# Kernel tuning notes

Hardware: AMD Instinct MI355X
Metric: run time of the kernel (lower is better)

The kernel has to match this reference:

```python
import jax, jax.numpy as jnp
import numpy as np

N = 50000      # nodes
E = 800000     # edges (avg degree 16)
F_IN = 128     # num_features
HID = 128      # hidden_channels
C = 4          # num_labeled_classes


def setup_inputs() -> dict:
    key = jax.random.key(0)
    ks = jax.random.split(key, 12)
    x = jax.random.normal(ks[0], (N, F_IN), dtype=jnp.float32)
    edge_index = jax.random.randint(ks[1], (2, E), 0, N, dtype=jnp.int32)

    def lin(k, fan_in, fan_out):
        return (jax.random.normal(k, (fan_in, fan_out), dtype=jnp.float32)
                / np.float32(np.sqrt(fan_in)))

    return {
        "x": x,
        "edge_index": edge_index,
        # layer 0: SAGEConv(F_IN, HID) -> lin_l (with bias) on aggregated neighbors, lin_r on self
        "Wl0": lin(ks[2], F_IN, HID), "bl0": jnp.zeros((HID,), jnp.float32), "Wr0": lin(ks[3], F_IN, HID),
        # layer 1: SAGEConv(HID, HID)
        "Wl1": lin(ks[4], HID, HID), "bl1": jnp.zeros((HID,), jnp.float32), "Wr1": lin(ks[5], HID, HID),
        # layer 2: SAGEConv(HID, C)
        "Wl2": lin(ks[6], HID, C), "bl2": jnp.zeros((C,), jnp.float32), "Wr2": lin(ks[7], HID, C),
    }


def _sage_conv(x, src, dst, inv_deg, Wl, bl, Wr):
    # gather neighbor features [E, d], mean-aggregate at destination nodes
    msg = x[src]
    agg = jax.ops.segment_sum(msg, dst, num_segments=N)  # [N, d]
    mean = agg * inv_deg[:, None]
    # out = lin_l(mean_j) + lin_r(x_i)   (PyG SAGEConv default, mean aggr)
    return mean @ Wl + bl + x @ Wr


def reference(x, edge_index, Wl0, bl0, Wr0, Wl1, bl1, Wr1, Wl2, bl2, Wr2):
    src = edge_index[0]
    dst = edge_index[1]
    # in-degree of each destination node, clamped to 1 (isolated nodes -> 0 mean)
    deg = jax.ops.segment_sum(jnp.ones((E,), x.dtype), dst, num_segments=N)
    inv_deg = jnp.where(deg > 0, 1.0 / jnp.maximum(deg, 1.0), 0.0)

    h = _sage_conv(x, src, dst, inv_deg, Wl0, bl0, Wr0)
    h = jax.nn.relu(h)
    # dropout(p=0.5) is identity in eval mode
    h2 = _sage_conv(h, src, dst, inv_deg, Wl1, bl1, Wr1)
    out = _sage_conv(h2, src, dst, inv_deg, Wl2, bl2, Wr2)
    return (out, out, h2)
```

## Files before the change

### kernel.cpp

```cpp
#include <hip/hip_runtime.h>
#include <hip/hip_bf16.h>
#include <stdint.h>

#define NNODES 50000
#define NEDGES 800000
#define FDIM   128
#define NCLS   4
#define NB     196
#define ECAP   6144
#define LPITCH 136
#define NPH    8

typedef uint32_t u32;
typedef unsigned short u16;
typedef __bf16 bf16x8 __attribute__((ext_vector_type(8)));
typedef float f32x4 __attribute__((ext_vector_type(4)));

__device__ __forceinline__ u16 f2bf(float f) {
    u32 u = __float_as_uint(f);
    u32 r = u + 0x7fffu + ((u >> 16) & 1u);
    return (u16)(r >> 16);
}
__device__ __forceinline__ u32 pack2(float a, float b) {
    return (u32)f2bf(a) | ((u32)f2bf(b) << 16);
}
__device__ __forceinline__ float bflo(u32 p) { return __uint_as_float(p << 16); }
__device__ __forceinline__ float bfhi(u32 p) { return __uint_as_float(p & 0xffff0000u); }

__global__ void k_bhist(const int* __restrict__ dst, int* __restrict__ bcnt) {
    __shared__ int h[NB];
    int t = threadIdx.x;
    if (t < NB) h[t] = 0;
    __syncthreads();
    int base = blockIdx.x * 1024;
#pragma unroll
    for (int i = 0; i < 4; ++i) {
        int e = base + i * 256 + t;
        if (e < NEDGES) atomicAdd(&h[dst[e] >> 8], 1);
    }
    __syncthreads();
    if (t < NB) {
        int v = h[t];
        if (v) atomicAdd(&bcnt[t], v);
    }
}

__global__ void k_bscan(const int* __restrict__ bcnt, int* __restrict__ boffs,
                        int* __restrict__ bcur) {
    int t = threadIdx.x;
    int v = (t < NB) ? bcnt[t] : 0;
    __shared__ int s[256];
    s[t] = v;
    __syncthreads();
    for (int off = 1; off < 256; off <<= 1) {
        int u = (t >= off) ? s[t - off] : 0;
        __syncthreads();
        s[t] += u;
        __syncthreads();
    }
    if (t < NB) { int ex = s[t] - v; boffs[t] = ex; bcur[t] = ex; }
    if (t == 0) boffs[NB] = NEDGES;
}

__global__ void k_bscatter(const int* __restrict__ src, const int* __restrict__ dst,
                           int* __restrict__ bcur, u32* __restrict__ ebuf) {
    __shared__ int h[NB];
    __shared__ int base[NB];
    int t = threadIdx.x;
    if (t < NB) h[t] = 0;
    __syncthreads();
    int eb = blockIdx.x * 1024;
    int mb[4];
    u32 pk[4];
#pragma unroll
    for (int i = 0; i < 4; ++i) {
        int e = eb + i * 256 + t;
        if (e < NEDGES) {
            int d = dst[e];
            mb[i] = d >> 8;
            pk[i] = (u32)src[e] | ((u32)d << 16);
            atomicAdd(&h[mb[i]], 1);
        } else mb[i] = -1;
    }
    __syncthreads();
    if (t < NB) {
        int v = h[t];
        base[t] = v ? atomicAdd(&bcur[t], v) : 0;
        h[t] = 0;
    }
    __syncthreads();
#pragma unroll
    for (int i = 0; i < 4; ++i) {
        if (mb[i] >= 0) {
            int r = atomicAdd(&h[mb[i]], 1);
            ebuf[base[mb[i]] + r] = pk[i];
        }
    }
}

__global__ void __launch_bounds__(256) k_bfinal(
        const u32* __restrict__ ebuf, const int* __restrict__ boffs,
        int* __restrict__ offs, float* __restrict__ invd, int* __restrict__ csr) {
    __shared__ u32 se[ECAP];
    __shared__ int deg8[256 * NPH];
    __shared__ int s[256];
    int b = blockIdx.x, t = threadIdx.x;
    int nbase = b << 8;
    int ebeg = boffs[b], eend = boffs[b + 1];
    int ecnt = eend - ebeg;
#pragma unroll
    for (int j = 0; j < NPH; ++j) deg8[t * NPH + j] = 0;
    __syncthreads();
    for (int i = t; i < ecnt; i += 256) {
        u32 e = ebuf[ebeg + i];
        if (i < ECAP) se[i] = e;
        int dl = (int)(e >> 16) - nbase;
        int ph = (int)(e & 0xffffu) >> 13;
        atomicAdd(&deg8[dl * NPH + ph], 1);
    }
    __syncthreads();
    int pre[NPH];
    int run = 0;
#pragma unroll
    for (int j = 0; j < NPH; ++j) { pre[j] = run; run += deg8[t * NPH + j]; }
    int d = run;
    s[t] = d;
    __syncthreads();
    for (int off = 1; off < 256; off <<= 1) {
        int u = (t >= off) ? s[t - off] : 0;
        __syncthreads();
        s[t] += u;
        __syncthreads();
    }
    int ex = s[t] - d;
    int node = nbase + t;
    if (node < NNODES) {
        offs[node] = ebeg + ex;
        invd[node] = (d > 0) ? (1.0f / (float)d) : 0.0f;
    }
    __syncthreads();
#pragma unroll
    for (int j = 0; j < NPH; ++j) deg8[t * NPH + j] = ex + pre[j];
    __syncthreads();
    for (int i = t; i < ecnt; i += 256) {
        u32 e = (i < ECAP) ? se[i] : ebuf[ebeg + i];
        int dl = (int)(e >> 16) - nbase;
        int sv = (int)(e & 0xffffu);
        int r = atomicAdd(&deg8[dl * NPH + (sv >> 13)], 1);
        csr[ebeg + r] = sv;
    }
    if (b == 0 && t == 0) offs[NNODES] = NEDGES;
}

__global__ void k_pack(const float* __restrict__ Wl, const float* __restrict__ Wr,
                       u16* __restrict__ Bp) {
    int tid = blockIdx.x * 256 + threadIdx.x;
    int j    = tid & 7;
    int lane = (tid >> 3) & 63;
    int ks   = (tid >> 9) & 3;
    int nt   = tid >> 11;
    int col  = nt * 16 + (lane & 15);
    int k    = ks * 32 + (lane >> 4) * 8 + j;
    float v = (col < FDIM) ? Wl[k * FDIM + col] : Wr[k * FDIM + (col - FDIM)];
    Bp[tid] = f2bf(v);
}

template <int INF32>
__global__ void __launch_bounds__(256) k_mfma(
        const void* __restrict__ in,
        const uint4* __restrict__ Bp,
        const float* __restrict__ bias,
        u16* __restrict__ y,
        u16* __restrict__ zb) {
    __shared__ u16 sA[64 * LPITCH];
    int t = threadIdx.x;
    int blk = blockIdx.x;
    int wave = t >> 6;
    int lane = t & 63;
    int m    = lane & 15;
    int quad = lane >> 4;

    {
        int row = t >> 2;
        int q   = t & 3;
        int r = blk * 64 + row;
        if (r >= NNODES) r = NNODES - 1;
        if (INF32) {
            const float4* gs = (const float4*)((const float*)in + (size_t)r * FDIM) + q * 8;
            uint4* ld = (uint4*)(sA + row * LPITCH + q * 32);
#pragma unroll
            for (int i = 0; i < 4; ++i) {
                float4 a = gs[2 * i], b = gs[2 * i + 1];
                uint4 v;
                v.x = pack2(a.x, a.y); v.y = pack2(a.z, a.w);
                v.z = pack2(b.x, b.y); v.w = pack2(b.z, b.w);
                ld[i] = v;
            }
        } else {
            const uint4* gsrc = (const uint4*)((const u16*)in + (size_t)r * FDIM);
            uint4* ldst = (uint4*)(sA + row * LPITCH);
#pragma unroll
            for (int i = 0; i < 4; ++i) ldst[q * 4 + i] = gsrc[q * 4 + i];
        }
    }

    uint4 breg[4][4];
#pragma unroll
    for (int ks = 0; ks < 4; ++ks)
#pragma unroll
        for (int nt = 0; nt < 4; ++nt)
            breg[ks][nt] = Bp[((wave * 4 + nt) * 4 + ks) * 64 + lane];

    __syncthreads();

    bf16x8 a[4][4];
#pragma unroll
    for (int mt = 0; mt < 4; ++mt)
#pragma unroll
        for (int ks = 0; ks < 4; ++ks) {
            const uint4* ap = (const uint4*)(sA + (mt * 16 + m) * LPITCH + ks * 32 + quad * 8);
            a[mt][ks] = __builtin_bit_cast(bf16x8, *ap);
        }

    f32x4 acc[4][4];
#pragma unroll
    for (int mt = 0; mt < 4; ++mt)
#pragma unroll
        for (int nt = 0; nt < 4; ++nt) acc[mt][nt] = (f32x4){0.f, 0.f, 0.f, 0.f};

#pragma unroll
    for (int ks = 0; ks < 4; ++ks)
#pragma unroll
        for (int nt = 0; nt < 4; ++nt) {
            bf16x8 b = __builtin_bit_cast(bf16x8, breg[ks][nt]);
#pragma unroll
            for (int mt = 0; mt < 4; ++mt)
                acc[mt][nt] = __builtin_amdgcn_mfma_f32_16x16x32_bf16(
                    a[mt][ks], b, acc[mt][nt], 0, 0, 0);
        }

    __syncthreads();
    if (wave < 2) {
#pragma unroll
        for (int nt = 0; nt < 4; ++nt) {
            int col = (wave * 4 + nt) * 16 + m;
#pragma unroll
            for (int mt = 0; mt < 4; ++mt)
#pragma unroll
                for (int r = 0; r < 4; ++r)
                    sA[(mt * 16 + quad * 4 + r) * LPITCH + col] = f2bf(acc[mt][nt][r]);
        }
    }
    __syncthreads();
#pragma unroll
    for (int i = 0; i < 4; ++i) {
        int g = i * 256 + t;
        int row = g >> 4, ch = g & 15;
        int gr = blk * 64 + row;
        if (gr < NNODES) {
            uint4 v = *(const uint4*)(sA + row * LPITCH + ch * 8);
            *((uint4*)(y + (size_t)gr * FDIM) + ch) = v;
        }
    }
    __syncthreads();
    if (wave >= 2) {
#pragma unroll
        for (int nt = 0; nt < 4; ++nt) {
            int col = (wave * 4 + nt) * 16 + m - 128;
            float bv = bias[col];
#pragma unroll
            for (int mt = 0; mt < 4; ++mt)
#pragma unroll
                for (int r = 0; r < 4; ++r)
                    sA[(mt * 16 + quad * 4 + r) * LPITCH + col] = f2bf(acc[mt][nt][r] + bv);
        }
    }
    __syncthreads();
#pragma unroll
    for (int i = 0; i < 4; ++i) {
        int g = i * 256 + t;
        int row = g >> 4, ch = g & 15;
        int gr = blk * 64 + row;
        if (gr < NNODES) {
            uint4 v = *(const uint4*)(sA + row * LPITCH + ch * 8);
            *((uint4*)(zb + (size_t)gr * FDIM) + ch) = v;
        }
    }
}

template <int RELU, int OUTBF>
__global__ void k_agg(const u16* __restrict__ y,
                      const int* __restrict__ offs,
                      const int* __restrict__ csr,
                      const float* __restrict__ invd,
                      const u16* __restrict__ zb,
                      u16* __restrict__ outb,
                      float* __restrict__ outf) {
    int t = threadIdx.x;
    int nl = t >> 4, q = t & 15;
    int n = blockIdx.x * 16 + nl;
    int beg = offs[n], end = offs[n + 1];
    float a0 = 0, a1 = 0, a2 = 0, a3 = 0, a4 = 0, a5 = 0, a6 = 0, a7 = 0;
    const u16* yq = y + (size_t)q * 8;
    for (int i = beg; i < end; ++i) {
        int s = csr[i];
        uint4 v = *(const uint4*)(yq + (size_t)s * FDIM);
        a0 += bflo(v.x); a1 += bfhi(v.x);
        a2 += bflo(v.y); a3 += bfhi(v.y);
        a4 += bflo(v.z); a5 += bfhi(v.z);
        a6 += bflo(v.w); a7 += bfhi(v.w);
    }
    float iv = invd[n];
    uint4 zv = *(const uint4*)(zb + (size_t)n * FDIM + q * 8);
    float r0 = fmaf(a0, iv, bflo(zv.x)), r1 = fmaf(a1, iv, bfhi(zv.x));
    float r2 = fmaf(a2, iv, bflo(zv.y)), r3 = fmaf(a3, iv, bfhi(zv.y));
    float r4 = fmaf(a4, iv, bflo(zv.z)), r5 = fmaf(a5, iv, bfhi(zv.z));
    float r6 = fmaf(a6, iv, bflo(zv.w)), r7 = fmaf(a7, iv, bfhi(zv.w));
    if (RELU) {
        r0 = fmaxf(r0, 0.f); r1 = fmaxf(r1, 0.f); r2 = fmaxf(r2, 0.f); r3 = fmaxf(r3, 0.f);
        r4 = fmaxf(r4, 0.f); r5 = fmaxf(r5, 0.f); r6 = fmaxf(r6, 0.f); r7 = fmaxf(r7, 0.f);
    }
    if (OUTBF) {
        uint4 o;
        o.x = pack2(r0, r1); o.y = pack2(r2, r3);
        o.z = pack2(r4, r5); o.w = pack2(r6, r7);
        *(uint4*)(outb + (size_t)n * FDIM + q * 8) = o;
    } else {
        float* o = outf + (size_t)n * FDIM + q * 8;
        ((float4*)o)[0] = make_float4(r0, r1, r2, r3);
        ((float4*)o)[1] = make_float4(r4, r5, r6, r7);
    }
}

__global__ void k_gemm4(const float* __restrict__ h2,
                        const float* __restrict__ Wl,
                        const float* __restrict__ Wr,
                        const float* __restrict__ bias,
                        float* __restrict__ y4,
                        float* __restrict__ outz) {
    int tid = blockIdx.x * blockDim.x + threadIdx.x;
    int n = tid >> 2, c = tid & 3;
    if (n >= NNODES) return;
    const float4* row = (const float4*)(h2 + (size_t)n * FDIM);
    float a = 0, b = 0;
#pragma unroll 8
    for (int k4 = 0; k4 < 32; ++k4) {
        float4 v = row[k4];
        int k = k4 * 4;
        a = fmaf(v.x, Wl[(k + 0) * 4 + c], a); b = fmaf(v.x, Wr[(k + 0) * 4 + c], b);
        a = fmaf(v.y, Wl[(k + 1) * 4 + c], a); b = fmaf(v.y, Wr[(k + 1) * 4 + c], b);
        a = fmaf(v.z, Wl[(k + 2) * 4 + c], a); b = fmaf(v.z, Wr[(k + 2) * 4 + c], b);
        a = fmaf(v.w, Wl[(k + 3) * 4 + c], a); b = fmaf(v.w, Wr[(k + 3) * 4 + c], b);
    }
    y4[(size_t)n * 4 + c] = a;
    outz[(size_t)n * 4 + c] = b + bias[c];
}

__global__ void k_agg4(const float* __restrict__ y4,
                       const int* __restrict__ offs,
                       const int* __restrict__ csr,
                       const float* __restrict__ invd,
                       float* __restrict__ out) {
    int tid = blockIdx.x * blockDim.x + threadIdx.x;
    int n = tid >> 2, c = tid & 3;
    if (n >= NNODES) return;
    int beg = offs[n], end = offs[n + 1];
    float acc = 0;
    for (int i = beg; i < end; ++i) acc += y4[(size_t)csr[i] * 4 + c];
    float r = fmaf(acc, invd[n], out[(size_t)n * 4 + c]);
    out[(size_t)n * 4 + c] = r;
    out[(size_t)NNODES * NCLS + (size_t)n * 4 + c] = r;
}

extern "C" void kernel_launch(void* const* d_in, const int* in_sizes, int n_in,
                              void* d_out, int out_size, void* d_ws, size_t ws_size,
                              hipStream_t stream) {
    const float* x   = (const float*)d_in[0];
    const int* ei    = (const int*)d_in[1];
    const float* Wl0 = (const float*)d_in[2];
    const float* bl0 = (const float*)d_in[3];
    const float* Wr0 = (const float*)d_in[4];
    const float* Wl1 = (const float*)d_in[5];
    const float* bl1 = (const float*)d_in[6];
    const float* Wr1 = (const float*)d_in[7];
    const float* Wl2 = (const float*)d_in[8];
    const float* bl2 = (const float*)d_in[9];
    const float* Wr2 = (const float*)d_in[10];

    const int* src = ei;
    const int* dst = ei + NEDGES;

    float* out = (float*)d_out;
    float* h2  = out + 2 * (size_t)NNODES * NCLS;

    char* ws = (char*)d_ws;
    int*   offs = (int*)(ws + 0);
    float* invd = (float*)(ws + 200192);
    int*   bcnt = (int*)(ws + 400384);
    int*   boffs= (int*)(ws + 401408);
    int*   bcur = (int*)(ws + 402432);
    int*   csr  = (int*)(ws + 403456);
    u16*   y    = (u16*)(ws + 3603456);
    u16*   hb   = (u16*)(ws + 16403456);
    u16*   zb   = (u16*)(ws + 29203456);
    u32*   ebuf = (u32*)zb;
    float* y4   = (float*)(ws + 42003456);
    u16*   Bp0  = (u16*)(ws + 42803456);
    u16*   Bp1  = (u16*)(ws + 42868992);

    hipMemsetAsync(bcnt, 0, NB * sizeof(int), stream);
    k_bhist<<<782, 256, 0, stream>>>(dst, bcnt);
    k_bscan<<<1, 256, 0, stream>>>(bcnt, boffs, bcur);
    k_bscatter<<<782, 256, 0, stream>>>(src, dst, bcur, ebuf);
    k_bfinal<<<NB, 256, 0, stream>>>(ebuf, boffs, offs, invd, csr);

    k_pack<<<128, 256, 0, stream>>>(Wl0, Wr0, Bp0);
    k_pack<<<128, 256, 0, stream>>>(Wl1, Wr1, Bp1);

    const int mfmaBlocks = (NNODES + 63) / 64;

    k_mfma<1><<<mfmaBlocks, 256, 0, stream>>>(x, (const uint4*)Bp0, bl0, y, zb);
    k_agg<1, 1><<<NNODES / 16, 256, 0, stream>>>(y, offs, csr, invd, zb, hb, nullptr);

    k_mfma<0><<<mfmaBlocks, 256, 0, stream>>>(hb, (const uint4*)Bp1, bl1, y, zb);
    k_agg<0, 0><<<NNODES / 16, 256, 0, stream>>>(y, offs, csr, invd, zb, nullptr, h2);

    k_gemm4<<<(NNODES * NCLS + 255) / 256, 256, 0, stream>>>(h2, Wl2, Wr2, bl2, y4, out);
    k_agg4<<<(NNODES * NCLS + 255) / 256, 256, 0, stream>>>(y4, offs, csr, invd, out);
}
```

Measured before the change: 284.6 us.

## Fuse preprocessing kernels, overlap edge scatter with layer-0 GEMM, fuse final projection

Merges the histogram and both weight-pack kernels into one launch. The bucket scan and edge scatter now run inside the same grid as the layer-0 MFMA GEMM, using block-index partitioning so the two can overlap. The bucket offsets are recomputed locally in k_bfinal instead of a separate scan kernel. The layer-2 projection (k_gemm4) is folded into the second aggregation kernel via per-row shuffle reductions, and neighbor indices are staged in shared memory. This cuts launch count and idle gaps but adds redundant per-block scans and a reworked workspace layout.

```diff
diff --git a/kernel.cpp b/kernel.cpp
--- a/kernel.cpp
+++ b/kernel.cpp
@@ -10,6 +10,7 @@
 #define ECAP   6144
 #define LPITCH 136
 #define NPH    8
+#define SCAP   768
 
 typedef uint32_t u32;
 typedef unsigned short u16;
@@ -27,166 +28,61 @@
 __device__ __forceinline__ float bflo(u32 p) { return __uint_as_float(p << 16); }
 __device__ __forceinline__ float bfhi(u32 p) { return __uint_as_float(p & 0xffff0000u); }
 
-__global__ void k_bhist(const int* __restrict__ dst, int* __restrict__ bcnt) {
-    __shared__ int h[NB];
+__global__ void __launch_bounds__(256) k_pre(
+        const int* __restrict__ dst,
+        const float* __restrict__ Wl0, const float* __restrict__ Wr0,
+        const float* __restrict__ Wl1, const float* __restrict__ Wr1,
+        int* __restrict__ bcnt, u16* __restrict__ Bp0, u16* __restrict__ Bp1) {
     int t = threadIdx.x;
-    if (t < NB) h[t] = 0;
-    __syncthreads();
-    int base = blockIdx.x * 1024;
-#pragma unroll
-    for (int i = 0; i < 4; ++i) {
-        int e = base + i * 256 + t;
-        if (e < NEDGES) atomicAdd(&h[dst[e] >> 8], 1);
-    }
-    __syncthreads();
-    if (t < NB) {
-        int v = h[t];
-        if (v) atomicAdd(&bcnt[t], v);
-    }
-}
-
-__global__ void k_bscan(const int* __restrict__ bcnt, int* __restrict__ boffs,
-                        int* __restrict__ bcur) {
-    int t = threadIdx.x;
-    int v = (t < NB) ? bcnt[t] : 0;
-    __shared__ int s[256];
-    s[t] = v;
-    __syncthreads();
-    for (int off = 1; off < 256; off <<= 1) {
-        int u = (t >= off) ? s[t - off] : 0;
-        __syncthreads();
-        s[t] += u;
-        __syncthreads();
-    }
-    if (t < NB) { int ex = s[t] - v; boffs[t] = ex; bcur[t] = ex; }
-    if (t == 0) boffs[NB] = NEDGES;
-}
-
-__global__ void k_bscatter(const int* __restrict__ src, const int* __restrict__ dst,
-                           int* __restrict__ bcur, u32* __restrict__ ebuf) {
-    __shared__ int h[NB];
-    __shared__ int base[NB];
-    int t = threadIdx.x;
-    if (t < NB) h[t] = 0;
-    __syncthreads();
-    int eb = blockIdx.x * 1024;
-    int mb[4];
-    u32 pk[4];
-#pragma unroll
-    for (int i = 0; i < 4; ++i) {
-        int e = eb + i * 256 + t;
-        if (e < NEDGES) {
-            int d = dst[e];
-            mb[i] = d >> 8;
-            pk[i] = (u32)src[e] | ((u32)d << 16);
-            atomicAdd(&h[mb[i]], 1);
-        } else mb[i] = -1;
-    }
-    __syncthreads();
-    if (t < NB) {
-        int v = h[t];
-        base[t] = v ? atomicAdd(&bcur[t], v) : 0;
-        h[t] = 0;
-    }
-    __syncthreads();
-#pragma unroll
-    for (int i = 0; i < 4; ++i) {
-        if (mb[i] >= 0) {
-            int r = atomicAdd(&h[mb[i]], 1);
-            ebuf[base[mb[i]] + r] = pk[i];
-        }
-    }
-}
-
-__global__ void __launch_bounds__(256) k_bfinal(
-        const u32* __restrict__ ebuf, const int* __restrict__ boffs,
-        int* __restrict__ offs, float* __restrict__ invd, int* __restrict__ csr) {
-    __shared__ u32 se[ECAP];
-    __shared__ int deg8[256 * NPH];
-    __shared__ int s[256];
-    int b = blockIdx.x, t = threadIdx.x;
-    int nbase = b << 8;
-    int ebeg = boffs[b], eend = boffs[b + 1];
-    int ecnt = eend - ebeg;
-#pragma unroll
-    for (int j = 0; j < NPH; ++j) deg8[t * NPH + j] = 0;
-    __syncthreads();
-    for (int i = t; i < ecnt; i += 256) {
-        u32 e = ebuf[ebeg + i];
-        if (i < ECAP) se[i] = e;
-        int dl = (int)(e >> 16) - nbase;
-        int ph = (int)(e & 0xffffu) >> 13;
-        atomicAdd(&deg8[dl * NPH + ph], 1);
-    }
-    __syncthreads();
-    int pre[NPH];
-    int run = 0;
-#pragma unroll
-    for (int j = 0; j < NPH; ++j) { pre[j] = run; run += deg8[t * NPH + j]; }
-    int d = run;
-    s[t] = d;
-    __syncthreads();
-    for (int off = 1; off < 256; off <<= 1) {
-        int u = (t >= off) ? s[t - off] : 0;
-        __syncthreads();
-        s[t] += u;
-        __syncthreads();
-    }
-    int ex = s[t] - d;
-    int node = nbase + t;
-    if (node < NNODES) {
-        offs[node] = ebeg + ex;
-        invd[node] = (d > 0) ? (1.0f / (float)d) : 0.0f;
-    }
-    __syncthreads();
-#pragma unroll
-    for (int j = 0; j < NPH; ++j) deg8[t * NPH + j] = ex + pre[j];
-    __syncthreads();
-    for (int i = t; i < ecnt; i += 256) {
-        u32 e = (i < ECAP) ? se[i] : ebuf[ebeg + i];
-        int dl = (int)(e >> 16) - nbase;
-        int sv = (int)(e & 0xffffu);
-        int r = atomicAdd(&deg8[dl * NPH + (sv >> 13)], 1);
-        csr[ebeg + r] = sv;
-    }
-    if (b == 0 && t == 0) offs[NNODES] = NEDGES;
-}
-
-__global__ void k_pack(const float* __restrict__ Wl, const float* __restrict__ Wr,
-                       u16* __restrict__ Bp) {
-    int tid = blockIdx.x * 256 + threadIdx.x;
-    int j    = tid & 7;
-    int lane = (tid >> 3) & 63;
-    int ks   = (tid >> 9) & 3;
-    int nt   = tid >> 11;
-    int col  = nt * 16 + (lane & 15);
-    int k    = ks * 32 + (lane >> 4) * 8 + j;
-    float v = (col < FDIM) ? Wl[k * FDIM + col] : Wr[k * FDIM + (col - FDIM)];
-    Bp[tid] = f2bf(v);
-}
-
-template <int INF32>
-__global__ void __launch_bounds__(256) k_mfma(
-        const void* __restrict__ in,
-        const uint4* __restrict__ Bp,
-        const float* __restrict__ bias,
-        u16* __restrict__ y,
-        u16* __restrict__ zb) {
+    int bid = blockIdx.x;
+    if (bid < 782) {
+        __shared__ int h[NB];
+        if (t < NB) h[t] = 0;
+        __syncthreads();
+        int base = bid * 1024;
+#pragma unroll
+        for (int i = 0; i < 4; ++i) {
+            int e = base + i * 256 + t;
+            if (e < NEDGES) atomicAdd(&h[dst[e] >> 8], 1);
+        }
+        __syncthreads();
+        if (t < NB) {
+            int v = h[t];
+            if (v) atomicAdd(&bcnt[t], v);
+        }
+    } else {
+        int layer = (bid < 910) ? 0 : 1;
+        int pid = bid - (layer ? 910 : 782);
+        int tid = pid * 256 + t;
+        int j    = tid & 7;
+        int lane = (tid >> 3) & 63;
+        int ks   = (tid >> 9) & 3;
+        int nt   = tid >> 11;
+        int col  = nt * 16 + (lane & 15);
+        int k    = ks * 32 + (lane >> 4) * 8 + j;
+        const float* Wl = layer ? Wl1 : Wl0;
+        const float* Wr = layer ? Wr1 : Wr0;
+        float v = (col < FDIM) ? Wl[k * FDIM + col] : Wr[k * FDIM + (col - FDIM)];
+        (layer ? Bp1 : Bp0)[tid] = f2bf(v);
+    }
+}
+
+__global__ void __launch_bounds__(256) k_scatmfma(
+        const float* __restrict__ x, const uint4* __restrict__ Bp,
+        const float* __restrict__ bias, u16* __restrict__ y, u16* __restrict__ zb,
+        const int* __restrict__ src, const int* __restrict__ dst,
+        const int* __restrict__ bcnt, int* __restrict__ bcur,
+        u32* __restrict__ ebuf) {
     __shared__ u16 sA[64 * LPITCH];
     int t = threadIdx.x;
-    int blk = blockIdx.x;
-    int wave = t >> 6;
-    int lane = t & 63;
-    int m    = lane & 15;
-    int quad = lane >> 4;
-
-    {
-        int row = t >> 2;
-        int q   = t & 3;
-        int r = blk * 64 + row;
-        if (r >= NNODES) r = NNODES - 1;
-        if (INF32) {
-            const float4* gs = (const float4*)((const float*)in + (size_t)r * FDIM) + q * 8;
+    if (blockIdx.x < 782) {
+        int blk = blockIdx.x;
+        int wave = t >> 6, lane = t & 63, m = lane & 15, quad = lane >> 4;
+        {
+            int row = t >> 2, q = t & 3;
+            int r = blk * 64 + row;
+            if (r >= NNODES) r = NNODES - 1;
+            const float4* gs = (const float4*)(x + (size_t)r * FDIM) + q * 8;
             uint4* ld = (uint4*)(sA + row * LPITCH + q * 32);
 #pragma unroll
             for (int i = 0; i < 4; ++i) {
@@ -196,114 +92,210 @@
                 v.z = pack2(b.x, b.y); v.w = pack2(b.z, b.w);
                 ld[i] = v;
             }
-        } else {
-            const uint4* gsrc = (const uint4*)((const u16*)in + (size_t)r * FDIM);
-            uint4* ldst = (uint4*)(sA + row * LPITCH);
-#pragma unroll
-            for (int i = 0; i < 4; ++i) ldst[q * 4 + i] = gsrc[q * 4 + i];
-        }
-    }
-
-    uint4 breg[4][4];
-#pragma unroll
-    for (int ks = 0; ks < 4; ++ks)
-#pragma unroll
-        for (int nt = 0; nt < 4; ++nt)
-            breg[ks][nt] = Bp[((wave * 4 + nt) * 4 + ks) * 64 + lane];
-
-    __syncthreads();
-
-    bf16x8 a[4][4];
-#pragma unroll
-    for (int mt = 0; mt < 4; ++mt)
-#pragma unroll
-        for (int ks = 0; ks < 4; ++ks) {
-            const uint4* ap = (const uint4*)(sA + (mt * 16 + m) * LPITCH + ks * 32 + quad * 8);
-            a[mt][ks] = __builtin_bit_cast(bf16x8, *ap);
-        }
-
-    f32x4 acc[4][4];
-#pragma unroll
-    for (int mt = 0; mt < 4; ++mt)
-#pragma unroll
-        for (int nt = 0; nt < 4; ++nt) acc[mt][nt] = (f32x4){0.f, 0.f, 0.f, 0.f};
-
-#pragma unroll
-    for (int ks = 0; ks < 4; ++ks)
-#pragma unroll
-        for (int nt = 0; nt < 4; ++nt) {
-            bf16x8 b = __builtin_bit_cast(bf16x8, breg[ks][nt]);
-#pragma unroll
-            for (int mt = 0; mt < 4; ++mt)
-                acc[mt][nt] = __builtin_amdgcn_mfma_f32_16x16x32_bf16(
-                    a[mt][ks], b, acc[mt][nt], 0, 0, 0);
-        }
-
-    __syncthreads();
-    if (wave < 2) {
-#pragma unroll
-        for (int nt = 0; nt < 4; ++nt) {
-            int col = (wave * 4 + nt) * 16 + m;
-#pragma unroll
-            for (int mt = 0; mt < 4; ++mt)
-#pragma unroll
-                for (int r = 0; r < 4; ++r)
-                    sA[(mt * 16 + quad * 4 + r) * LPITCH + col] = f2bf(acc[mt][nt][r]);
-        }
-    }
-    __syncthreads();
-#pragma unroll
-    for (int i = 0; i < 4; ++i) {
-        int g = i * 256 + t;
-        int row = g >> 4, ch = g & 15;
-        int gr = blk * 64 + row;
-        if (gr < NNODES) {
-            uint4 v = *(const uint4*)(sA + row * LPITCH + ch * 8);
-            *((uint4*)(y + (size_t)gr * FDIM) + ch) = v;
-        }
-    }
-    __syncthreads();
-    if (wave >= 2) {
-#pragma unroll
-        for (int nt = 0; nt < 4; ++nt) {
-            int col = (wave * 4 + nt) * 16 + m - 128;
-            float bv = bias[col];
-#pragma unroll
-            for (int mt = 0; mt < 4; ++mt)
-#pragma unroll
-                for (int r = 0; r < 4; ++r)
-                    sA[(mt * 16 + quad * 4 + r) * LPITCH + col] = f2bf(acc[mt][nt][r] + bv);
-        }
-    }
-    __syncthreads();
-#pragma unroll
-    for (int i = 0; i < 4; ++i) {
-        int g = i * 256 + t;
-        int row = g >> 4, ch = g & 15;
-        int gr = blk * 64 + row;
-        if (gr < NNODES) {
-            uint4 v = *(const uint4*)(sA + row * LPITCH + ch * 8);
-            *((uint4*)(zb + (size_t)gr * FDIM) + ch) = v;
-        }
-    }
-}
-
-template <int RELU, int OUTBF>
-__global__ void k_agg(const u16* __restrict__ y,
-                      const int* __restrict__ offs,
-                      const int* __restrict__ csr,
-                      const float* __restrict__ invd,
-                      const u16* __restrict__ zb,
-                      u16* __restrict__ outb,
-                      float* __restrict__ outf) {
+        }
+        uint4 breg[4][4];
+#pragma unroll
+        for (int ks = 0; ks < 4; ++ks)
+#pragma unroll
+            for (int nt = 0; nt < 4; ++nt)
+                breg[ks][nt] = Bp[((wave * 4 + nt) * 4 + ks) * 64 + lane];
+        __syncthreads();
+        bf16x8 a[4][4];
+#pragma unroll
+        for (int mt = 0; mt < 4; ++mt)
+#pragma unroll
+            for (int ks = 0; ks < 4; ++ks)
+                a[mt][ks] = __builtin_bit_cast(bf16x8,
+                    *(const uint4*)(sA + (mt * 16 + m) * LPITCH + ks * 32 + quad * 8));
+        f32x4 acc[4][4];
+#pragma unroll
+        for (int mt = 0; mt < 4; ++mt)
+#pragma unroll
+            for (int nt = 0; nt < 4; ++nt) acc[mt][nt] = (f32x4){0.f, 0.f, 0.f, 0.f};
+#pragma unroll
+        for (int ks = 0; ks < 4; ++ks)
+#pragma unroll
+            for (int nt = 0; nt < 4; ++nt) {
+                bf16x8 b = __builtin_bit_cast(bf16x8, breg[ks][nt]);
+#pragma unroll
+                for (int mt = 0; mt < 4; ++mt)
+                    acc[mt][nt] = __builtin_amdgcn_mfma_f32_16x16x32_bf16(
+                        a[mt][ks], b, acc[mt][nt], 0, 0, 0);
+            }
+        __syncthreads();
+        if (wave < 2) {
+#pragma unroll
+            for (int nt = 0; nt < 4; ++nt) {
+                int col = (wave * 4 + nt) * 16 + m;
+#pragma unroll
+                for (int mt = 0; mt < 4; ++mt)
+#pragma unroll
+                    for (int r = 0; r < 4; ++r)
+                        sA[(mt * 16 + quad * 4 + r) * LPITCH + col] = f2bf(acc[mt][nt][r]);
+            }
+        }
+        __syncthreads();
+#pragma unroll
+        for (int i = 0; i < 4; ++i) {
+            int g = i * 256 + t, row = g >> 4, ch = g & 15;
+            int gr = blk * 64 + row;
+            if (gr < NNODES)
+                *((uint4*)(y + (size_t)gr * FDIM) + ch) =
+                    *(const uint4*)(sA + row * LPITCH + ch * 8);
+        }
+        __syncthreads();
+        if (wave >= 2) {
+#pragma unroll
+            for (int nt = 0; nt < 4; ++nt) {
+                int col = (wave * 4 + nt) * 16 + m - 128;
+                float bv = bias[col];
+#pragma unroll
+                for (int mt = 0; mt < 4; ++mt)
+#pragma unroll
+                    for (int r = 0; r < 4; ++r)
+                        sA[(mt * 16 + quad * 4 + r) * LPITCH + col] = f2bf(acc[mt][nt][r] + bv);
+            }
+        }
+        __syncthreads();
+#pragma unroll
+        for (int i = 0; i < 4; ++i) {
+            int g = i * 256 + t, row = g >> 4, ch = g & 15;
+            int gr = blk * 64 + row;
+            if (gr < NNODES)
+                *((uint4*)(zb + (size_t)gr * FDIM) + ch) =
+                    *(const uint4*)(sA + row * LPITCH + ch * 8);
+        }
+    } else {
+        int* hh = (int*)sA;
+        int* bb = hh + 256;
+        int* ss = bb + 256;
+        int v = (t < NB) ? bcnt[t] : 0;
+        ss[t] = v;
+        __syncthreads();
+        for (int off = 1; off < 256; off <<= 1) {
+            int u = (t >= off) ? ss[t - off] : 0;
+            __syncthreads();
+            ss[t] += u;
+            __syncthreads();
+        }
+        int boff = ss[t] - v;
+        hh[t] = 0;
+        __syncthreads();
+        int eb = (blockIdx.x - 782) * 1024;
+        int mb[4];
+        u32 pk[4];
+#pragma unroll
+        for (int i = 0; i < 4; ++i) {
+            int e = eb + i * 256 + t;
+            if (e < NEDGES) {
+                int d = dst[e];
+                mb[i] = d >> 8;
+                pk[i] = (u32)src[e] | ((u32)d << 16);
+                atomicAdd(&hh[mb[i]], 1);
+            } else mb[i] = -1;
+        }
+        __syncthreads();
+        if (t < NB) {
+            int c = hh[t];
+            bb[t] = c ? (boff + atomicAdd(&bcur[t], c)) : 0;
+            hh[t] = 0;
+        }
+        __syncthreads();
+#pragma unroll
+        for (int i = 0; i < 4; ++i) {
+            if (mb[i] >= 0) {
+                int r = atomicAdd(&hh[mb[i]], 1);
+                ebuf[bb[mb[i]] + r] = pk[i];
+            }
+        }
+    }
+}
+
+__global__ void __launch_bounds__(256) k_bfinal(
+        const u32* __restrict__ ebuf, const int* __restrict__ bcnt,
+        int* __restrict__ offs, float* __restrict__ invd, int* __restrict__ csr) {
+    __shared__ u32 se[ECAP];
+    __shared__ int deg8[256 * NPH];
+    __shared__ int s[256];
+    int b = blockIdx.x, t = threadIdx.x;
+    int nbase = b << 8;
+    int v = (t < NB) ? bcnt[t] : 0;
+    s[t] = v;
+    __syncthreads();
+    for (int off = 1; off < 256; off <<= 1) {
+        int u = (t >= off) ? s[t - off] : 0;
+        __syncthreads();
+        s[t] += u;
+        __syncthreads();
+    }
+    int ebeg = s[b] - bcnt[b];
+    int ecnt = bcnt[b];
+    __syncthreads();
+#pragma unroll
+    for (int j = 0; j < NPH; ++j) deg8[t * NPH + j] = 0;
+    __syncthreads();
+    for (int i = t; i < ecnt; i += 256) {
+        u32 e = ebuf[ebeg + i];
+        if (i < ECAP) se[i] = e;
+        atomicAdd(&deg8[((int)(e >> 16) - nbase) * NPH + (((int)(e & 0xffffu)) >> 13)], 1);
+    }
+    __syncthreads();
+    int pre[NPH];
+    int run = 0;
+#pragma unroll
+    for (int j = 0; j < NPH; ++j) { pre[j] = run; run += deg8[t * NPH + j]; }
+    int d = run;
+    s[t] = d;
+    __syncthreads();
+    for (int off = 1; off < 256; off <<= 1) {
+        int u = (t >= off) ? s[t - off] : 0;
+        __syncthreads();
+        s[t] += u;
+        __syncthreads();
+    }
+    int ex = s[t] - d;
+    int node = nbase + t;
+    if (node < NNODES) {
+        offs[node] = ebeg + ex;
+        invd[node] = (d > 0) ? (1.0f / (float)d) : 0.0f;
+    }
+    __syncthreads();
+#pragma unroll
+    for (int j = 0; j < NPH; ++j) deg8[t * NPH + j] = ex + pre[j];
+    __syncthreads();
+    for (int i = t; i < ecnt; i += 256) {
+        u32 e = (i < ECAP) ? se[i] : ebuf[ebeg + i];
+        int dl = (int)(e >> 16) - nbase;
+        int sv = (int)(e & 0xffffu);
+        int r = atomicAdd(&deg8[dl * NPH + (sv >> 13)], 1);
+        csr[ebeg + r] = sv;
+    }
+    if (b == 0 && t == 0) offs[NNODES] = NEDGES;
+}
+
+template <int RELU, int OUTBF, int FUSE4>
+__global__ void __launch_bounds__(256) k_agg(
+        const u16* __restrict__ y, const int* __restrict__ offs,
+        const int* __restrict__ csr, const float* __restrict__ invd,
+        const u16* __restrict__ zb, u16* __restrict__ outb, float* __restrict__ outf,
+        const float* __restrict__ Wl2, const float* __restrict__ Wr2,
+        const float* __restrict__ bl2, float* __restrict__ y4,
+        float* __restrict__ outz) {
+    __shared__ int sidx[SCAP];
     int t = threadIdx.x;
+    int n0 = blockIdx.x * 16;
+    int base0 = offs[n0];
+    int ecnt = offs[n0 + 16] - base0;
+    for (int i = t; i < ecnt && i < SCAP; i += 256) sidx[i] = csr[base0 + i];
+    __syncthreads();
     int nl = t >> 4, q = t & 15;
-    int n = blockIdx.x * 16 + nl;
+    int n = n0 + nl;
     int beg = offs[n], end = offs[n + 1];
     float a0 = 0, a1 = 0, a2 = 0, a3 = 0, a4 = 0, a5 = 0, a6 = 0, a7 = 0;
     const u16* yq = y + (size_t)q * 8;
-    for (int i = beg; i < end; ++i) {
-        int s = csr[i];
+    for (int ii = beg; ii < end; ++ii) {
+        int li = ii - base0;
+        int s = (li < SCAP) ? sidx[li] : csr[ii];
         uint4 v = *(const uint4*)(yq + (size_t)s * FDIM);
         a0 += bflo(v.x); a1 += bfhi(v.x);
         a2 += bflo(v.y); a3 += bfhi(v.y);
@@ -330,30 +322,125 @@
         ((float4*)o)[0] = make_float4(r0, r1, r2, r3);
         ((float4*)o)[1] = make_float4(r4, r5, r6, r7);
     }
-}
-
-__global__ void k_gemm4(const float* __restrict__ h2,
-                        const float* __restrict__ Wl,
-                        const float* __restrict__ Wr,
-                        const float* __restrict__ bias,
-                        float* __restrict__ y4,
-                        float* __restrict__ outz) {
-    int tid = blockIdx.x * blockDim.x + threadIdx.x;
-    int n = tid >> 2, c = tid & 3;
-    if (n >= NNODES) return;
-    const float4* row = (const float4*)(h2 + (size_t)n * FDIM);
-    float a = 0, b = 0;
-#pragma unroll 8
-    for (int k4 = 0; k4 < 32; ++k4) {
-        float4 v = row[k4];
-        int k = k4 * 4;
-        a = fmaf(v.x, Wl[(k + 0) * 4 + c], a); b = fmaf(v.x, Wr[(k + 0) * 4 + c], b);
-        a = fmaf(v.y, Wl[(k + 1) * 4 + c], a); b = fmaf(v.y, Wr[(k + 1) * 4 + c], b);
-        a = fmaf(v.z, Wl[(k + 2) * 4 + c], a); b = fmaf(v.z, Wr[(k + 2) * 4 + c], b);
-        a = fmaf(v.w, Wl[(k + 3) * 4 + c], a); b = fmaf(v.w, Wr[(k + 3) * 4 + c], b);
-    }
-    y4[(size_t)n * 4 + c] = a;
-    outz[(size_t)n * 4 + c] = b + bias[c];
+    if (FUSE4) {
+        float rr[8] = {r0, r1, r2, r3, r4, r5, r6, r7};
+        float4 py = {0, 0, 0, 0}, pz = {0, 0, 0, 0};
+        const float4* wl4 = (const float4*)Wl2;
+        const float4* wr4 = (const float4*)Wr2;
+#pragma unroll
+        for (int j = 0; j < 8; ++j) {
+            float4 wl = wl4[q * 8 + j], wr = wr4[q * 8 + j];
+            py.x += rr[j] * wl.x; py.y += rr[j] * wl.y;
+            py.z += rr[j] * wl.z; py.w += rr[j] * wl.w;
+            pz.x += rr[j] * wr.x; pz.y += rr[j] * wr.y;
+            pz.z += rr[j] * wr.z; pz.w += rr[j] * wr.w;
+        }
+#pragma unroll
+        for (int off = 1; off < 16; off <<= 1) {
+            py.x += __shfl_xor(py.x, off, 16); py.y += __shfl_xor(py.y, off, 16);
+            py.z += __shfl_xor(py.z, off, 16); py.w += __shfl_xor(py.w, off, 16);
+            pz.x += __shfl_xor(pz.x, off, 16); pz.y += __shfl_xor(pz.y, off, 16);
+            pz.z += __shfl_xor(pz.z, off, 16); pz.w += __shfl_xor(pz.w, off, 16);
+        }
+        if (q == 0) {
+            ((float4*)y4)[n] = py;
+            float4 b2 = *(const float4*)bl2;
+            float4 o;
+            o.x = pz.x + b2.x; o.y = pz.y + b2.y;
+            o.z = pz.z + b2.z; o.w = pz.w + b2.w;
+            ((float4*)outz)[n] = o;
+        }
+    }
+}
+
+__global__ void __launch_bounds__(256) k_mfma1(
+        const u16* __restrict__ in, const uint4* __restrict__ Bp,
+        const float* __restrict__ bias, u16* __restrict__ y, u16* __restrict__ zb) {
+    __shared__ u16 sA[64 * LPITCH];
+    int t = threadIdx.x;
+    int blk = blockIdx.x;
+    int wave = t >> 6, lane = t & 63, m = lane & 15, quad = lane >> 4;
+    {
+        int row = t >> 2, q = t & 3;
+        int r = blk * 64 + row;
+        if (r >= NNODES) r = NNODES - 1;
+        const uint4* gsrc = (const uint4*)(in + (size_t)r * FDIM);
+        uint4* ldst = (uint4*)(sA + row * LPITCH);
+#pragma unroll
+        for (int i = 0; i < 4; ++i) ldst[q * 4 + i] = gsrc[q * 4 + i];
+    }
+    uint4 breg[4][4];
+#pragma unroll
+    for (int ks = 0; ks < 4; ++ks)
+#pragma unroll
+        for (int nt = 0; nt < 4; ++nt)
+            breg[ks][nt] = Bp[((wave * 4 + nt) * 4 + ks) * 64 + lane];
+    __syncthreads();
+    bf16x8 a[4][4];
+#pragma unroll
+    for (int mt = 0; mt < 4; ++mt)
+#pragma unroll
+        for (int ks = 0; ks < 4; ++ks)
+            a[mt][ks] = __builtin_bit_cast(bf16x8,
+                *(const uint4*)(sA + (mt * 16 + m) * LPITCH + ks * 32 + quad * 8));
+    f32x4 acc[4][4];
+#pragma unroll
+    for (int mt = 0; mt < 4; ++mt)
+#pragma unroll
+        for (int nt = 0; nt < 4; ++nt) acc[mt][nt] = (f32x4){0.f, 0.f, 0.f, 0.f};
+#pragma unroll
+    for (int ks = 0; ks < 4; ++ks)
+#pragma unroll
+        for (int nt = 0; nt < 4; ++nt) {
+            bf16x8 b = __builtin_bit_cast(bf16x8, breg[ks][nt]);
+#pragma unroll
+            for (int mt = 0; mt < 4; ++mt)
+                acc[mt][nt] = __builtin_amdgcn_mfma_f32_16x16x32_bf16(
+                    a[mt][ks], b, acc[mt][nt], 0, 0, 0);
+        }
+    __syncthreads();
+    if (wave < 2) {
+#pragma unroll
+        for (int nt = 0; nt < 4; ++nt) {
+            int col = (wave * 4 + nt) * 16 + m;
+#pragma unroll
+            for (int mt = 0; mt < 4; ++mt)
+#pragma unroll
+                for (int r = 0; r < 4; ++r)
+                    sA[(mt * 16 + quad * 4 + r) * LPITCH + col] = f2bf(acc[mt][nt][r]);
+        }
+    }
+    __syncthreads();
+#pragma unroll
+    for (int i = 0; i < 4; ++i) {
+        int g = i * 256 + t, row = g >> 4, ch = g & 15;
+        int gr = blk * 64 + row;
+        if (gr < NNODES)
+            *((uint4*)(y + (size_t)gr * FDIM) + ch) =
+                *(const uint4*)(sA + row * LPITCH + ch * 8);
+    }
+    __syncthreads();
+    if (wave >= 2) {
+#pragma unroll
+        for (int nt = 0; nt < 4; ++nt) {
+            int col = (wave * 4 + nt) * 16 + m - 128;
+            float bv = bias[col];
+#pragma unroll
+            for (int mt = 0; mt < 4; ++mt)
+#pragma unroll
+                for (int r = 0; r < 4; ++r)
+                    sA[(mt * 16 + quad * 4 + r) * LPITCH + col] = f2bf(acc[mt][nt][r] + bv);
+        }
+    }
+    __syncthreads();
+#pragma unroll
+    for (int i = 0; i < 4; ++i) {
+        int g = i * 256 + t, row = g >> 4, ch = g & 15;
+        int gr = blk * 64 + row;
+        if (gr < NNODES)
+            *((uint4*)(zb + (size_t)gr * FDIM) + ch) =
+                *(const uint4*)(sA + row * LPITCH + ch * 8);
+    }
 }
 
 __global__ void k_agg4(const float* __restrict__ y4,
@@ -397,34 +484,34 @@
     int*   offs = (int*)(ws + 0);
     float* invd = (float*)(ws + 200192);
     int*   bcnt = (int*)(ws + 400384);
-    int*   boffs= (int*)(ws + 401408);
-    int*   bcur = (int*)(ws + 402432);
-    int*   csr  = (int*)(ws + 403456);
-    u16*   y    = (u16*)(ws + 3603456);
-    u16*   hb   = (u16*)(ws + 16403456);
-    u16*   zb   = (u16*)(ws + 29203456);
-    u32*   ebuf = (u32*)zb;
-    float* y4   = (float*)(ws + 42003456);
-    u16*   Bp0  = (u16*)(ws + 42803456);
-    u16*   Bp1  = (u16*)(ws + 42868992);
-
-    hipMemsetAsync(bcnt, 0, NB * sizeof(int), stream);
-    k_bhist<<<782, 256, 0, stream>>>(dst, bcnt);
-    k_bscan<<<1, 256, 0, stream>>>(bcnt, boffs, bcur);
-    k_bscatter<<<782, 256, 0, stream>>>(src, dst, bcur, ebuf);
-    k_bfinal<<<NB, 256, 0, stream>>>(ebuf, boffs, offs, invd, csr);
-
-    k_pack<<<128, 256, 0, stream>>>(Wl0, Wr0, Bp0);
-    k_pack<<<128, 256, 0, stream>>>(Wl1, Wr1, Bp1);
-
-    const int mfmaBlocks = (NNODES + 63) / 64;
-
-    k_mfma<1><<<mfmaBlocks, 256, 0, stream>>>(x, (const uint4*)Bp0, bl0, y, zb);
-    k_agg<1, 1><<<NNODES / 16, 256, 0, stream>>>(y, offs, csr, invd, zb, hb, nullptr);
-
-    k_mfma<0><<<mfmaBlocks, 256, 0, stream>>>(hb, (const uint4*)Bp1, bl1, y, zb);
-    k_agg<0, 0><<<NNODES / 16, 256, 0, stream>>>(y, offs, csr, invd, zb, nullptr, h2);
-
-    k_gemm4<<<(NNODES * NCLS + 255) / 256, 256, 0, stream>>>(h2, Wl2, Wr2, bl2, y4, out);
+    int*   bcur = (int*)(ws + 401408);
+    int*   csr  = (int*)(ws + 402432);
+    u16*   y    = (u16*)(ws + 3602432);
+    u16*   hb   = (u16*)(ws + 16402432);
+    u16*   zb   = (u16*)(ws + 29202432);
+    u32*   ebuf = (u32*)hb;
+    float* y4   = (float*)(ws + 42002432);
+    u16*   Bp0  = (u16*)(ws + 42802432);
+    u16*   Bp1  = (u16*)(ws + 42867968);
+
+    hipMemsetAsync(bcnt, 0, 2048, stream);
+
+    k_pre<<<1038, 256, 0, stream>>>(dst, Wl0, Wr0, Wl1, Wr1, bcnt, Bp0, Bp1);
+
+    k_scatmfma<<<1564, 256, 0, stream>>>(x, (const uint4*)Bp0, bl0, y, zb,
+                                         src, dst, bcnt, bcur, ebuf);
+
+    k_bfinal<<<NB, 256, 0, stream>>>(ebuf, bcnt, offs, invd, csr);
+
+    k_agg<1, 1, 0><<<NNODES / 16, 256, 0, stream>>>(
+        y, offs, csr, invd, zb, hb, nullptr,
+        nullptr, nullptr, nullptr, nullptr, nullptr);
+
+    k_mfma1<<<(NNODES + 63) / 64, 256, 0, stream>>>(hb, (const uint4*)Bp1, bl1, y, zb);
+
+    k_agg<0, 0, 1><<<NNODES / 16, 256, 0, stream>>>(
+        y, offs, csr, invd, zb, nullptr, h2,
+        Wl2, Wr2, bl2, y4, out);
+
     k_agg4<<<(NNODES * NCLS + 255) / 256, 256, 0, stream>>>(y4, offs, csr, invd, out);
 }
```

Result: faster. 260.0 us (-8.6%).
